# Performance work log

Measured on AMD Instinct MI355X. Metric: run time of the kernel, lower is better.

Reference implementation:

```python
import jax, jax.numpy as jnp
import numpy as np

B, S, E = 8, 2048, 2048

def setup_inputs() -> dict:
    key = jax.random.key(0)
    k1, k2, k3, k4 = jax.random.split(key, 4)
    return {
        "batch_size": B,
        "seq_len": S,
        "embedding_dim": E,
        "time_decay": jax.random.normal(k1, (E,), dtype=jnp.float32),
        "time_first": jax.random.normal(k2, (E,), dtype=jnp.float32),
        "k": jax.random.normal(k3, (B, S, E), dtype=jnp.float32),
        "v": jax.random.normal(k4, (B, S, E), dtype=jnp.float32),
    }

def _wkv(time_decay, time_first, k, v):
    dtype = k.dtype
    b, s, e = k.shape
    # time-major for scan: [S, B, E]
    k_t = jnp.transpose(k, (1, 0, 2))
    v_t = jnp.transpose(v, (1, 0, 2))
    tf = time_first[None, :]  # [1, E] broadcast over batch
    td = time_decay[None, :]
    aa0 = jnp.zeros((b, e), dtype=dtype)
    bb0 = jnp.zeros((b, e), dtype=dtype)
    eps0 = jnp.zeros((b, e), dtype=dtype)  # MIN_VAL = 0.0

    def step(carry, kv):
        aa, bb, eps = carry
        kt, vt = kv
        e_tf_k = jnp.exp(tf + kt - eps)
        y_t = (aa + vt * e_tf_k) / (bb + e_tf_k)
        eps_next = jnp.maximum(td + eps, kt)
        e_td_k = jnp.exp(td + eps - eps_next)
        e_k = jnp.exp(kt - eps_next)
        aa = aa * e_td_k + vt * e_k
        bb = bb * e_td_k + e_k
        return (aa, bb, eps_next), y_t

    _, y_t = jax.lax.scan(step, (aa0, bb0, eps0), (k_t, v_t))
    return jnp.transpose(y_t, (1, 0, 2))  # [B, S, E]

def reference(batch_size, seq_len, embedding_dim, time_decay, time_first, k, v):
    return _wkv(time_decay, time_first, k, v)
```

## Files before the change

### kernel.cpp

```cpp
#include <hip/hip_runtime.h>


#define WKV_B 8
#define WKV_S 2048
#define WKV_E 2048

constexpr int U = 32;

__global__ __launch_bounds__(64) void wkv_scan_kernel(
    const float* __restrict__ td_g, const float* __restrict__ tf_g,
    const float* __restrict__ k_g, const float* __restrict__ v_g,
    float* __restrict__ y_g)
{
    constexpr int S = WKV_S;
    constexpr int E = WKV_E;

    const int c = blockIdx.x * 64 + threadIdx.x;
    const int b = c >> 11;
    const int e = c & (E - 1);

    const float td = td_g[e];
    const float tf = tf_g[e];

    const long base = (long)b * S * E + e;
    const float* __restrict__ kp = k_g + base;
    const float* __restrict__ vp = v_g + base;
    float* __restrict__ yp = y_g + base;

    float aa = 0.0f, bb = 0.0f, eps = 0.0f;

    float kA[U], vA[U], kB[U], vB[U];

#pragma unroll
    for (int i = 0; i < U; ++i) {
        kA[i] = __builtin_nontemporal_load(&kp[i * E]);
        vA[i] = __builtin_nontemporal_load(&vp[i * E]);
    }

    auto step = [&](float kt, float vt, int t) {
        const float e1 = __expf(tf + kt - eps);
        const float y  = __fdividef(fmaf(vt, e1, aa), bb + e1);
        __builtin_nontemporal_store(y, &yp[t * E]);
        const float tde  = td + eps;
        const float eps2 = fmaxf(tde, kt);
        const float e2   = __expf(tde - eps2);
        const float e3   = __expf(kt - eps2);
        aa = fmaf(aa, e2, vt * e3);
        bb = fmaf(bb, e2, e3);
        eps = eps2;
    };

    for (int t0 = 0; t0 < S; t0 += 2 * U) {
#pragma unroll
        for (int i = 0; i < U; ++i) {
            kB[i] = __builtin_nontemporal_load(&kp[(t0 + U + i) * E]);
            vB[i] = __builtin_nontemporal_load(&vp[(t0 + U + i) * E]);
        }
#pragma unroll
        for (int i = 0; i < U; ++i) step(kA[i], vA[i], t0 + i);

        if (t0 + 2 * U < S) {
#pragma unroll
            for (int i = 0; i < U; ++i) {
                kA[i] = __builtin_nontemporal_load(&kp[(t0 + 2 * U + i) * E]);
                vA[i] = __builtin_nontemporal_load(&vp[(t0 + 2 * U + i) * E]);
            }
        }
#pragma unroll
        for (int i = 0; i < U; ++i) step(kB[i], vB[i], t0 + U + i);
    }
}

extern "C" void kernel_launch(void* const* d_in, const int* in_sizes, int n_in,
                              void* d_out, int out_size, void* d_ws, size_t ws_size,
                              hipStream_t stream) {
    const float* td = (const float*)d_in[3];
    const float* tf = (const float*)d_in[4];
    const float* k  = (const float*)d_in[5];
    const float* v  = (const float*)d_in[6];
    float* y        = (float*)d_out;
    (void)in_sizes; (void)n_in; (void)out_size; (void)d_ws; (void)ws_size;

    dim3 grid((WKV_B * WKV_E) / 64);
    dim3 block(64);
    hipLaunchKernelGGL(wkv_scan_kernel, grid, block, 0, stream, td, tf, k, v, y);
}
```

Baseline: 432.0 us.

## Split WKV scan into chunked three-pass parallel scan over sequence

Replaces the single sequential scan per channel with a chunked scan. Pass 1 computes a per-chunk state over 16 chunks, pass 2 combines chunk states serially with a CL*td decay, and pass 3 rescans each chunk from its prefix state and writes outputs. This exposes far more parallelism than the 256 single-wave blocks of the original. The cost is reading k/v almost twice and two extra launches. A single-pass fallback runs if workspace is too small.

After: 372.9 us. 13.7% less time.

```diff
diff --git a/kernel.cpp b/kernel.cpp
--- a/kernel.cpp
+++ b/kernel.cpp
@@ -1,73 +1,170 @@
 #include <hip/hip_runtime.h>
 
 
-#define WKV_B 8
-#define WKV_S 2048
-#define WKV_E 2048
+#define B_ 8
+#define S_ 2048
+#define E_ 2048
+constexpr int BE = B_ * E_;
+constexpr int CH = 16;
+constexpr int CL = S_ / CH;
 
-constexpr int U = 32;
+__global__ __launch_bounds__(64) void wkv_pass1(
+    const float* __restrict__ td_g,
+    const float* __restrict__ k_g, const float* __restrict__ v_g,
+    float* __restrict__ sa, float* __restrict__ sb, float* __restrict__ se)
+{
+    const int gid = blockIdx.x * 64 + threadIdx.x;
+    const int j = gid >> 14;
+    const int c = gid & (BE - 1);
+    const int b = c >> 11;
+    const int e = c & (E_ - 1);
+    const float td = td_g[e];
+    const long base = (long)b * S_ * E_ + (long)(j * CL) * E_ + e;
+    const float* __restrict__ kp = k_g + base;
+    const float* __restrict__ vp = v_g + base;
 
-__global__ __launch_bounds__(64) void wkv_scan_kernel(
+    float aa = 0.f, bb = 0.f, eps = 0.f;
+    constexpr int U = 8;
+    float kA[U], vA[U], kB[U], vB[U];
+#pragma unroll
+    for (int i = 0; i < U; ++i) { kA[i] = kp[i * E_]; vA[i] = vp[i * E_]; }
+
+    auto st = [&](float kt, float vt) {
+        const float tde = td + eps;
+        const float m   = fmaxf(tde, kt);
+        const float p   = __expf(tde - m);
+        const float q   = __expf(kt - m);
+        aa = fmaf(aa, p, vt * q);
+        bb = fmaf(bb, p, q);
+        eps = m;
+    };
+
+    for (int t0 = 0; t0 < CL; t0 += 2 * U) {
+#pragma unroll
+        for (int i = 0; i < U; ++i) { kB[i] = kp[(t0 + U + i) * E_]; vB[i] = vp[(t0 + U + i) * E_]; }
+#pragma unroll
+        for (int i = 0; i < U; ++i) st(kA[i], vA[i]);
+        if (t0 + 2 * U < CL) {
+#pragma unroll
+            for (int i = 0; i < U; ++i) { kA[i] = kp[(t0 + 2*U + i) * E_]; vA[i] = vp[(t0 + 2*U + i) * E_]; }
+        }
+#pragma unroll
+        for (int i = 0; i < U; ++i) st(kB[i], vB[i]);
+    }
+    sa[j * BE + c] = aa;
+    sb[j * BE + c] = bb;
+    se[j * BE + c] = eps;
+}
+
+__global__ __launch_bounds__(64) void wkv_pass2(
+    const float* __restrict__ td_g,
+    const float* __restrict__ sa, const float* __restrict__ sb, const float* __restrict__ se,
+    float* __restrict__ ia, float* __restrict__ ib, float* __restrict__ ie)
+{
+    const int c = blockIdx.x * 64 + threadIdx.x;
+    const int e = c & (E_ - 1);
+    const float Ltd = (float)CL * td_g[e];
+
+    float aa = 0.f, bb = 0.f, eps = 0.f;
+    ia[c] = 0.f; ib[c] = 0.f; ie[c] = 0.f;
+#pragma unroll
+    for (int j = 1; j < CH; ++j) {
+        const float a_c = sa[(j - 1) * BE + c];
+        const float b_c = sb[(j - 1) * BE + c];
+        const float e_c = se[(j - 1) * BE + c];
+        const float ed  = eps + Ltd;
+        const float ne  = fmaxf(ed, e_c);
+        const float f1  = __expf(ed - ne);
+        const float f2  = __expf(e_c - ne);
+        aa = aa * f1 + a_c * f2;
+        bb = bb * f1 + b_c * f2;
+        eps = ne;
+        ia[j * BE + c] = aa;
+        ib[j * BE + c] = bb;
+        ie[j * BE + c] = eps;
+    }
+}
+
+__global__ __launch_bounds__(64) void wkv_pass3(
+    const float* __restrict__ td_g, const float* __restrict__ tf_g,
+    const float* __restrict__ k_g, const float* __restrict__ v_g,
+    const float* __restrict__ ia, const float* __restrict__ ib, const float* __restrict__ ie,
+    float* __restrict__ y_g)
+{
+    const int gid = blockIdx.x * 64 + threadIdx.x;
+    const int j = gid >> 14;
+    const int c = gid & (BE - 1);
+    const int b = c >> 11;
+    const int e = c & (E_ - 1);
+    const float td = td_g[e];
+    const float tf = tf_g[e];
+    const long base = (long)b * S_ * E_ + (long)(j * CL) * E_ + e;
+    const float* __restrict__ kp = k_g + base;
+    const float* __restrict__ vp = v_g + base;
+    float* __restrict__ yp = y_g + base;
+
+    float aa = ia[j * BE + c];
+    float bb = ib[j * BE + c];
+    float eps = ie[j * BE + c];
+
+    constexpr int U = 8;
+    float kA[U], vA[U], kB[U], vB[U];
+#pragma unroll
+    for (int i = 0; i < U; ++i) { kA[i] = kp[i * E_]; vA[i] = vp[i * E_]; }
+
+    auto st = [&](float kt, float vt, int t) {
+        const float e1 = __expf(tf + kt - eps);
+        const float y  = __fdividef(fmaf(vt, e1, aa), bb + e1);
+        __builtin_nontemporal_store(y, &yp[t * E_]);
+        const float tde = td + eps;
+        const float m   = fmaxf(tde, kt);
+        const float p   = __expf(tde - m);
+        const float q   = __expf(kt - m);
+        aa = fmaf(aa, p, vt * q);
+        bb = fmaf(bb, p, q);
+        eps = m;
+    };
+
+    for (int t0 = 0; t0 < CL; t0 += 2 * U) {
+#pragma unroll
+        for (int i = 0; i < U; ++i) { kB[i] = kp[(t0 + U + i) * E_]; vB[i] = vp[(t0 + U + i) * E_]; }
+#pragma unroll
+        for (int i = 0; i < U; ++i) st(kA[i], vA[i], t0 + i);
+        if (t0 + 2 * U < CL) {
+#pragma unroll
+            for (int i = 0; i < U; ++i) { kA[i] = kp[(t0 + 2*U + i) * E_]; vA[i] = vp[(t0 + 2*U + i) * E_]; }
+        }
+#pragma unroll
+        for (int i = 0; i < U; ++i) st(kB[i], vB[i], t0 + U + i);
+    }
+}
+
+__global__ __launch_bounds__(64) void wkv_single(
     const float* __restrict__ td_g, const float* __restrict__ tf_g,
     const float* __restrict__ k_g, const float* __restrict__ v_g,
     float* __restrict__ y_g)
 {
-    constexpr int S = WKV_S;
-    constexpr int E = WKV_E;
-
     const int c = blockIdx.x * 64 + threadIdx.x;
     const int b = c >> 11;
-    const int e = c & (E - 1);
-
+    const int e = c & (E_ - 1);
     const float td = td_g[e];
     const float tf = tf_g[e];
-
-    const long base = (long)b * S * E + e;
+    const long base = (long)b * S_ * E_ + e;
     const float* __restrict__ kp = k_g + base;
     const float* __restrict__ vp = v_g + base;
     float* __restrict__ yp = y_g + base;
-
-    float aa = 0.0f, bb = 0.0f, eps = 0.0f;
-
-    float kA[U], vA[U], kB[U], vB[U];
-
-#pragma unroll
-    for (int i = 0; i < U; ++i) {
-        kA[i] = __builtin_nontemporal_load(&kp[i * E]);
-        vA[i] = __builtin_nontemporal_load(&vp[i * E]);
-    }
-
-    auto step = [&](float kt, float vt, int t) {
+    float aa = 0.f, bb = 0.f, eps = 0.f;
+    for (int t = 0; t < S_; ++t) {
+        const float kt = kp[t * E_], vt = vp[t * E_];
         const float e1 = __expf(tf + kt - eps);
-        const float y  = __fdividef(fmaf(vt, e1, aa), bb + e1);
-        __builtin_nontemporal_store(y, &yp[t * E]);
-        const float tde  = td + eps;
-        const float eps2 = fmaxf(tde, kt);
-        const float e2   = __expf(tde - eps2);
-        const float e3   = __expf(kt - eps2);
-        aa = fmaf(aa, e2, vt * e3);
-        bb = fmaf(bb, e2, e3);
-        eps = eps2;
-    };
-
-    for (int t0 = 0; t0 < S; t0 += 2 * U) {
-#pragma unroll
-        for (int i = 0; i < U; ++i) {
-            kB[i] = __builtin_nontemporal_load(&kp[(t0 + U + i) * E]);
-            vB[i] = __builtin_nontemporal_load(&vp[(t0 + U + i) * E]);
-        }
-#pragma unroll
-        for (int i = 0; i < U; ++i) step(kA[i], vA[i], t0 + i);
-
-        if (t0 + 2 * U < S) {
-#pragma unroll
-            for (int i = 0; i < U; ++i) {
-                kA[i] = __builtin_nontemporal_load(&kp[(t0 + 2 * U + i) * E]);
-                vA[i] = __builtin_nontemporal_load(&vp[(t0 + 2 * U + i) * E]);
-            }
-        }
-#pragma unroll
-        for (int i = 0; i < U; ++i) step(kB[i], vB[i], t0 + U + i);
+        yp[t * E_] = __fdividef(fmaf(vt, e1, aa), bb + e1);
+        const float tde = td + eps;
+        const float m = fmaxf(tde, kt);
+        const float p = __expf(tde - m);
+        const float q = __expf(kt - m);
+        aa = fmaf(aa, p, vt * q);
+        bb = fmaf(bb, p, q);
+        eps = m;
     }
 }
 
@@ -79,9 +176,24 @@
     const float* k  = (const float*)d_in[5];
     const float* v  = (const float*)d_in[6];
     float* y        = (float*)d_out;
-    (void)in_sizes; (void)n_in; (void)out_size; (void)d_ws; (void)ws_size;
+    (void)in_sizes; (void)n_in; (void)out_size;
 
-    dim3 grid((WKV_B * WKV_E) / 64);
-    dim3 block(64);
-    hipLaunchKernelGGL(wkv_scan_kernel, grid, block, 0, stream, td, tf, k, v, y);
+    const size_t arr = (size_t)CH * BE * sizeof(float);
+    if (ws_size < 6 * arr) {
+        hipLaunchKernelGGL(wkv_single, dim3(BE / 64), dim3(64), 0, stream, td, tf, k, v, y);
+        return;
+    }
+    float* sa = (float*)d_ws;
+    float* sb = sa + CH * BE;
+    float* se = sb + CH * BE;
+    float* ia = se + CH * BE;
+    float* ib = ia + CH * BE;
+    float* ie = ib + CH * BE;
+
+    hipLaunchKernelGGL(wkv_pass1, dim3((CH - 1) * BE / 64), dim3(64), 0, stream,
+                       td, k, v, sa, sb, se);
+    hipLaunchKernelGGL(wkv_pass2, dim3(BE / 64), dim3(64), 0, stream,
+                       td, sa, sb, se, ia, ib, ie);
+    hipLaunchKernelGGL(wkv_pass3, dim3(CH * BE / 64), dim3(64), 0, stream,
+                       td, tf, k, v, ia, ib, ie, y);
 }
```
